# Optimization experiments

Hardware: AMD Instinct MI355X
Metric: run time of the kernel (lower is better)

Reference implementation:

```python
import jax, jax.numpy as jnp
import numpy as np

N = 4096
NODE_DIM = 256
HIDDEN = 64
N_CLASSES = 16
N_HEADS = 4
NEG_SLOPE = 0.01  # F.leaky_relu default


def _xavier(key, shape):
    fan_out, fan_in = shape[0], shape[1]
    limit = float(np.sqrt(6.0 / (fan_in + fan_out)))
    return jax.random.uniform(key, shape, jnp.float32, -limit, limit)


def setup_inputs() -> dict:
    key = jax.random.key(0)
    ks = jax.random.split(key, 8)
    x = jax.random.normal(ks[0], (N, NODE_DIM), jnp.float32)
    adj_mat = jax.random.randint(ks[1], (N, N), 0, 2, jnp.int32)
    # head-stacked layer-1 params
    W1 = _xavier(ks[2], (N_HEADS * HIDDEN, NODE_DIM)).reshape(N_HEADS, HIDDEN, NODE_DIM)
    a1_1 = _xavier(ks[3], (N_HEADS * HIDDEN, 1)).reshape(N_HEADS, HIDDEN)
    a2_1 = _xavier(ks[4], (N_HEADS * HIDDEN, 1)).reshape(N_HEADS, HIDDEN)
    # layer-2 params
    W2 = _xavier(ks[5], (N_CLASSES, N_HEADS * HIDDEN))
    a1_2 = _xavier(ks[6], (N_CLASSES, 1))[:, 0]
    a2_2 = _xavier(ks[7], (N_CLASSES, 1))[:, 0]
    return {"x": x, "adj_mat": adj_mat, "W1": W1, "a1_1": a1_1, "a2_1": a2_1,
            "W2": W2, "a1_2": a1_2, "a2_2": a2_2}


def _attention_layer(x, adj_f, W, a1, a2):
    # x: [N, in_dim], W: [out_dim, in_dim], a1/a2: [out_dim]
    h = x @ W.T                               # [N, d]
    f1 = h @ a1                               # [N]
    f2 = h @ a2                               # [N]
    e = jax.nn.leaky_relu(f1[:, None] + f2[None, :], NEG_SLOPE)  # [N, N]
    e = e * adj_f
    e = jnp.where(e == 0, -jnp.inf, e)        # faithful to torch.where(e==0, -inf, e)
    alpha = jax.nn.softmax(e, axis=1)         # [N, N]
    return alpha @ h                          # [N, d]


def reference(x, adj_mat, W1, a1_1, a2_1, W2, a1_2, a2_2):
    adj_f = adj_mat.astype(x.dtype)
    # layer 1: vmap over heads, concat along feature dim
    heads = jax.vmap(_attention_layer, in_axes=(None, None, 0, 0, 0))(
        x, adj_f, W1, a1_1, a2_1)              # [H, N, hidden]
    h = jnp.transpose(heads, (1, 0, 2)).reshape(N, N_HEADS * HIDDEN)
    h = jax.nn.elu(h)
    # dropout p=0.0 -> identity
    logits = _attention_layer(h, adj_f, W2, a1_2, a2_2)  # [N, n_classes]
    return logits
```

## Files before the change

### kernel.cpp

```cpp
#include <hip/hip_runtime.h>
#include <cstdint>

typedef __bf16 bf16x8 __attribute__((ext_vector_type(8)));
typedef float  f32x4  __attribute__((ext_vector_type(4)));

__device__ __forceinline__ void split8(const float* v, bf16x8& hi, bf16x8& lo) {
    union { bf16x8 v; __bf16 e[8]; } h, l;
    #pragma unroll
    for (int j = 0; j < 8; j++) {
        __bf16 hb = (__bf16)v[j];
        float  r  = v[j] - (float)hb;
        h.e[j] = hb; l.e[j] = (__bf16)r;
    }
    hi = h.v; lo = l.v;
}
__device__ __forceinline__ bf16x8 cvt8(const float* v) {
    union { bf16x8 v; __bf16 e[8]; } u;
    #pragma unroll
    for (int j = 0; j < 8; j++) u.e[j] = (__bf16)v[j];
    return u.v;
}
__device__ __forceinline__ void splitstore(unsigned short* ph, unsigned short* pl, float v) {
    __bf16 hb = (__bf16)v;
    float  r  = v - (float)hb;
    __bf16 lb = (__bf16)r;
    unsigned short hu, lu;
    __builtin_memcpy(&hu, &hb, 2); __builtin_memcpy(&lu, &lb, 2);
    *ph = hu; *pl = lu;
}
__device__ __forceinline__ unsigned short f2bfh(float v) {
    __bf16 hb = (__bf16)v; unsigned short hu;
    __builtin_memcpy(&hu, &hb, 2); return hu;
}

__global__ __launch_bounds__(256)
void kzero(float4* __restrict__ p) {
    p[blockIdx.x * 256 + threadIdx.x] = float4{0.f, 0.f, 0.f, 0.f};
}

__global__ __launch_bounds__(256)
void kpre(const int* __restrict__ adj, unsigned long long* __restrict__ bm64,
          const float* __restrict__ w1, const float* __restrict__ w2,
          unsigned short* __restrict__ w1h, unsigned short* __restrict__ w1l,
          unsigned short* __restrict__ w2h, unsigned short* __restrict__ w2l) {
    int bx = blockIdx.x, tid = threadIdx.x;
    if (bx < 8192) {
        int row = bx >> 1, jbase = (bx & 1) * 2048;
        int wave = tid >> 6, lane = tid & 63;
        const int* base = adj + (size_t)row * 4096 + jbase + wave * 512;
        unsigned long long* bmw = bm64 + row * 64 + (jbase >> 6) + wave * 8;
        #pragma unroll
        for (int it = 0; it < 8; it++) {
            int v = base[it * 64 + lane];
            unsigned long long mask = __ballot(v != 0);
            if (lane == 0) bmw[it] = mask;
        }
        return;
    }
    int e = ((bx - 8192) * 256 + tid) * 4;
    const float* src; unsigned short *dh, *dl;
    if (e < 65536) { src = w1 + e; dh = w1h + e; dl = w1l + e; }
    else { int e2 = e - 65536; src = w2 + e2; dh = w2h + e2; dl = w2l + e2; }
    #pragma unroll
    for (int j = 0; j < 4; j++) splitstore(dh + j, dl + j, src[j]);
}

__global__ __launch_bounds__(256)
void k1_gemm(const float* __restrict__ x,
             const unsigned short* __restrict__ w1h,
             const unsigned short* __restrict__ w1l,
             const float* __restrict__ a11, const float* __restrict__ a21,
             unsigned short* __restrict__ h1t_hi, float* __restrict__ fvals) {
    int tid = threadIdx.x, wave = tid >> 6, lane = tid & 63;
    int q = lane >> 4, m = lane & 15;
    int i0 = blockIdx.x * 16;
    int c0 = wave * 64;
    f32x4 acc[4] = {};
    #pragma unroll
    for (int k0 = 0; k0 < 256; k0 += 32) {
        bf16x8 ah, al;
        split8(x + (i0 + m) * 256 + k0 + q * 8, ah, al);
        #pragma unroll
        for (int ct = 0; ct < 4; ct++) {
            bf16x8 bh = *(const bf16x8*)(w1h + (c0 + ct * 16 + m) * 256 + k0 + q * 8);
            bf16x8 bl = *(const bf16x8*)(w1l + (c0 + ct * 16 + m) * 256 + k0 + q * 8);
            acc[ct] = __builtin_amdgcn_mfma_f32_16x16x32_bf16(ah, bh, acc[ct], 0, 0, 0);
            acc[ct] = __builtin_amdgcn_mfma_f32_16x16x32_bf16(al, bh, acc[ct], 0, 0, 0);
            acc[ct] = __builtin_amdgcn_mfma_f32_16x16x32_bf16(ah, bl, acc[ct], 0, 0, 0);
        }
    }
    float a1v[4], a2v[4];
    #pragma unroll
    for (int ct = 0; ct < 4; ct++) {
        a1v[ct] = a11[wave * 64 + ct * 16 + m];
        a2v[ct] = a21[wave * 64 + ct * 16 + m];
    }
    #pragma unroll
    for (int r = 0; r < 4; r++) {
        int i = i0 + q * 4 + r;
        float s1 = 0.f, s2 = 0.f;
        #pragma unroll
        for (int ct = 0; ct < 4; ct++) {
            int c = c0 + ct * 16 + m;
            h1t_hi[c * 4096 + i] = f2bfh(acc[ct][r]);
            s1 += acc[ct][r] * a1v[ct];
            s2 += acc[ct][r] * a2v[ct];
        }
        #pragma unroll
        for (int off = 1; off < 16; off <<= 1) {
            s1 += __shfl_xor(s1, off);
            s2 += __shfl_xor(s2, off);
        }
        if (m == 0) {
            fvals[wave * 4096 + i] = s1;
            fvals[16384 + wave * 4096 + i] = s2;
        }
    }
}

template<int NCT, int JLEN, bool ATOM>
__global__ __launch_bounds__(256)
void attn_kernel(const unsigned char* __restrict__ bmb,
                 const float* __restrict__ f1_all,
                 const float* __restrict__ f2_all,
                 const unsigned short* __restrict__ BTh_all,
                 float* __restrict__ pacc,
                 float* __restrict__ zacc,
                 int pstride) {
    constexpr int S    = JLEN / 32;
    constexpr int ST   = (S % 8 == 0) ? S + 4 : S;
    constexpr int PR   = S / 4;
    constexpr int NU4  = 128 * PR;
    constexpr int CR   = NCT * 16;
    constexpr int TSTR = 40;
    int tid = threadIdx.x, wave = tid >> 6, lane = tid & 63;
    int q = lane >> 4, m = lane & 15;
    int head = blockIdx.y;
    int i0 = blockIdx.x * 128;
    int jstart = blockIdx.z * JLEN;

    if (!ATOM) {
        pacc += (size_t)blockIdx.z * (size_t)(4096 * pstride);
        zacc += (size_t)blockIdx.z * (size_t)((NCT == 4 ? 4 : 1) * 4096);
    }

    __shared__ unsigned int ldsbm[128 * ST];
    __shared__ unsigned short ldsbt[2][CR * TSTR];

    const unsigned short* BTh = BTh_all + (size_t)head * CR * 4096;

    for (int c = tid; c < NU4; c += 256) {
        int row = c / PR, part = c % PR;
        uint4 v = *(const uint4*)(bmb + (size_t)(i0 + row) * 512 + (jstart >> 3) + part * 16);
        *(uint4*)&ldsbm[row * ST + part * 4] = v;
    }
    uint4 vstage;
    int sc = tid >> 2, sp = tid & 3;
    if (tid < CR * 4) {
        vstage = *(const uint4*)(BTh + (size_t)sc * 4096 + jstart + sp * 8);
        *(uint4*)&ldsbt[0][sc * TSTR + sp * 8] = vstage;
    }

    const float* f1 = f1_all + head * 4096;
    const float* f2 = f2_all + head * 4096;
    int col0 = head * CR;

    int r0 = wave * 32;
    float f1s0 = f1[i0 + r0 + m];
    float f1s1 = f1[i0 + r0 + 16 + m];

    f32x4 acc0[NCT] = {}, acc1[NCT] = {};
    float z0 = 0.f, z1 = 0.f;

    constexpr int NIT = JLEN / 32;
    for (int it = 0; it < NIT; it++) {
        __syncthreads();
        int jl = it * 32;
        if (it + 1 < NIT && tid < CR * 4)
            vstage = *(const uint4*)(BTh + (size_t)sc * 4096 + jstart + jl + 32 + sp * 8);

        unsigned int md0 = ldsbm[(r0 + m) * ST + (jl >> 5)];
        unsigned int md1 = ldsbm[(r0 + 16 + m) * ST + (jl >> 5)];
        const float4* f2p = (const float4*)(f2 + jstart + jl + q * 8);
        float4 fa = f2p[0], fb = f2p[1];
        float fv[8] = {fa.x, fa.y, fa.z, fa.w, fb.x, fb.y, fb.z, fb.w};
        float pv0[8], pv1[8];
        #pragma unroll
        for (int jj = 0; jj < 8; jj++) {
            int bit = q * 8 + jj;
            float s0 = f1s0 + fv[jj];
            float e0 = fmaxf(s0, 0.01f * s0);
            bool v0 = ((md0 >> bit) & 1u) && (s0 != 0.0f);
            float p0 = v0 ? __expf(e0) : 0.0f;
            z0 += p0; pv0[jj] = p0;
            float s1 = f1s1 + fv[jj];
            float e1 = fmaxf(s1, 0.01f * s1);
            bool v1 = ((md1 >> bit) & 1u) && (s1 != 0.0f);
            float p1 = v1 ? __expf(e1) : 0.0f;
            z1 += p1; pv1[jj] = p1;
        }
        bf16x8 ah0 = cvt8(pv0), ah1 = cvt8(pv1);
        int cur = it & 1;
        #pragma unroll
        for (int ct = 0; ct < NCT; ct++) {
            bf16x8 bh = *(const bf16x8*)&ldsbt[cur][(ct * 16 + m) * TSTR + q * 8];
            acc0[ct] = __builtin_amdgcn_mfma_f32_16x16x32_bf16(ah0, bh, acc0[ct], 0, 0, 0);
            acc1[ct] = __builtin_amdgcn_mfma_f32_16x16x32_bf16(ah1, bh, acc1[ct], 0, 0, 0);
        }
        if (it + 1 < NIT && tid < CR * 4)
            *(uint4*)&ldsbt[1 - cur][sc * TSTR + sp * 8] = vstage;
    }
    z0 += __shfl_xor(z0, 16); z0 += __shfl_xor(z0, 32);
    z1 += __shfl_xor(z1, 16); z1 += __shfl_xor(z1, 32);
    if (lane < 16) {
        if (ATOM) {
            atomicAdd(&zacc[head * 4096 + i0 + r0 + lane], z0);
            atomicAdd(&zacc[head * 4096 + i0 + r0 + 16 + lane], z1);
        } else {
            zacc[head * 4096 + i0 + r0 + lane] = z0;
            zacc[head * 4096 + i0 + r0 + 16 + lane] = z1;
        }
    }
    #pragma unroll
    for (int ct = 0; ct < NCT; ct++)
        #pragma unroll
        for (int r = 0; r < 4; r++) {
            int col = col0 + ct * 16 + m;
            int rowA = i0 + r0 + q * 4 + r;
            if (ATOM) {
                atomicAdd(&pacc[rowA * pstride + col], acc0[ct][r]);
                atomicAdd(&pacc[(rowA + 16) * pstride + col], acc1[ct][r]);
            } else {
                pacc[rowA * pstride + col] = acc0[ct][r];
                pacc[(rowA + 16) * pstride + col] = acc1[ct][r];
            }
        }
}

__global__ __launch_bounds__(256)
void fin1c(const float* __restrict__ pp, const float* __restrict__ zp, int nj,
           unsigned short* __restrict__ hh, unsigned short* __restrict__ hl) {
    int row = blockIdx.x, col = threadIdx.x;
    float s = 0.f;
    for (int jc = 0; jc < nj; jc++) s += pp[(size_t)jc * (4096 * 256) + row * 256 + col];
    int head = col >> 6;
    float zz = 0.f;
    for (int jc = 0; jc < nj; jc++) zz += zp[jc * (4 * 4096) + head * 4096 + row];
    float v = s / zz;
    v = (v > 0.f) ? v : (__expf(v) - 1.0f);
    splitstore(&hh[row * 256 + col], &hl[row * 256 + col], v);
}

__global__ __launch_bounds__(256)
void k3_layer2(const unsigned short* __restrict__ helu_hi,
               const unsigned short* __restrict__ helu_lo,
               const unsigned short* __restrict__ w2h,
               const unsigned short* __restrict__ w2l,
               const float* __restrict__ a12,
               const float* __restrict__ a22,
               unsigned short* __restrict__ h2t_hi,
               float* __restrict__ fq) {
    int tid = threadIdx.x, wave = tid >> 6, lane = tid & 63;
    int q = lane >> 4, m = lane & 15;
    int i0 = (blockIdx.x * 4 + wave) * 16;
    f32x4 acc = {};
    #pragma unroll
    for (int k0 = 0; k0 < 256; k0 += 32) {
        bf16x8 ah = *(const bf16x8*)(helu_hi + (i0 + m) * 256 + k0 + q * 8);
        bf16x8 al = *(const bf16x8*)(helu_lo + (i0 + m) * 256 + k0 + q * 8);
        bf16x8 bh = *(const bf16x8*)(w2h + m * 256 + k0 + q * 8);
        bf16x8 bl = *(const bf16x8*)(w2l + m * 256 + k0 + q * 8);
        acc = __builtin_amdgcn_mfma_f32_16x16x32_bf16(ah, bh, acc, 0, 0, 0);
        acc = __builtin_amdgcn_mfma_f32_16x16x32_bf16(al, bh, acc, 0, 0, 0);
        acc = __builtin_amdgcn_mfma_f32_16x16x32_bf16(ah, bl, acc, 0, 0, 0);
    }
    float a1v = a12[m], a2v = a22[m];
    #pragma unroll
    for (int r = 0; r < 4; r++) {
        float v = acc[r];
        int i = i0 + q * 4 + r;
        h2t_hi[m * 4096 + i] = f2bfh(v);
        float s1 = v * a1v, s2 = v * a2v;
        #pragma unroll
        for (int off = 1; off < 16; off <<= 1) {
            s1 += __shfl_xor(s1, off);
            s2 += __shfl_xor(s2, off);
        }
        if (m == 0) { fq[i] = s1; fq[4096 + i] = s2; }
    }
}

__global__ __launch_bounds__(256)
void fin2(const float* __restrict__ pp, const float* __restrict__ zp, int nj,
          float* __restrict__ out) {
    int idx = blockIdx.x * 256 + threadIdx.x;
    float s = 0.f;
    for (int jc = 0; jc < nj; jc++) s += pp[jc * 65536 + idx];
    float zz = 0.f;
    for (int jc = 0; jc < nj; jc++) zz += zp[jc * 4096 + (idx >> 4)];
    out[idx] = s / zz;
}

extern "C" void kernel_launch(void* const* d_in, const int* in_sizes, int n_in,
                              void* d_out, int out_size, void* d_ws, size_t ws_size,
                              hipStream_t stream) {
    const float* x   = (const float*)d_in[0];
    const int*   adj = (const int*)d_in[1];
    const float* w1  = (const float*)d_in[2];
    const float* a11 = (const float*)d_in[3];
    const float* a21 = (const float*)d_in[4];
    const float* w2  = (const float*)d_in[5];
    const float* a12 = (const float*)d_in[6];
    const float* a22 = (const float*)d_in[7];
    float* out = (float*)d_out;

    uint8_t* w = (uint8_t*)d_ws;
    unsigned long long* bm  = (unsigned long long*)(w);
    unsigned short* h1t_hi  = (unsigned short*)(w + (2u << 20));
    unsigned short* h2t_hi  = (unsigned short*)(w + (4u << 20));
    float*          fvals   = (float*)(w + (4u << 20) + (128u << 10));
    float*          fq      = (float*)(w + (4u << 20) + (256u << 10));
    unsigned short* w1h     = (unsigned short*)(w + (4u << 20) + (288u << 10));
    unsigned short* w1l     = (unsigned short*)(w + (4u << 20) + (416u << 10));
    unsigned short* w2h     = (unsigned short*)(w + (4u << 20) + (544u << 10));
    unsigned short* w2l     = (unsigned short*)(w + (4u << 20) + (552u << 10));
    unsigned short* helu_hi = (unsigned short*)(w + (4u << 20) + (560u << 10));
    unsigned short* helu_lo = (unsigned short*)(w + (4u << 20) + (2608u << 10));

    bool big = ws_size >= ((size_t)48 << 20);
    float* p1 = (float*)(w + (9u << 20));
    float *z1, *p2, *z2;
    if (big) {
        z1 = p1 + (size_t)8 * 4096 * 256;
        p2 = z1 + 8 * 4 * 4096;
        z2 = p2 + (size_t)16 * 4096 * 16;
    } else {
        z1 = p1 + 4096 * 256;
        p2 = z1 + 4 * 4096;
        z2 = p2 + 4096 * 16;
    }

    if (!big) kzero<<<1108, 256, 0, stream>>>((float4*)p1);
    kpre<<<8260, 256, 0, stream>>>(adj, bm, w1, w2, w1h, w1l, w2h, w2l);
    k1_gemm<<<256, 256, 0, stream>>>(x, w1h, w1l, a11, a21, h1t_hi, fvals);
    if (big)
        attn_kernel<4, 512, false><<<dim3(32, 4, 8), 256, 0, stream>>>(
            (const unsigned char*)bm, fvals, fvals + 16384, h1t_hi, p1, z1, 256);
    else
        attn_kernel<4, 512, true><<<dim3(32, 4, 8), 256, 0, stream>>>(
            (const unsigned char*)bm, fvals, fvals + 16384, h1t_hi, p1, z1, 256);
    fin1c<<<4096, 256, 0, stream>>>(p1, z1, big ? 8 : 1, helu_hi, helu_lo);
    k3_layer2<<<64, 256, 0, stream>>>(helu_hi, helu_lo, w2h, w2l, a12, a22,
                                      h2t_hi, fq);
    if (big)
        attn_kernel<1, 256, false><<<dim3(32, 1, 16), 256, 0, stream>>>(
            (const unsigned char*)bm, fq, fq + 4096, h2t_hi, p2, z2, 16);
    else
        attn_kernel<1, 256, true><<<dim3(32, 1, 16), 256, 0, stream>>>(
            (const unsigned char*)bm, fq, fq + 4096, h2t_hi, p2, z2, 16);
    fin2<<<256, 256, 0, stream>>>(p2, z2, big ? 16 : 1, out);
}
```

Measured before the change: 201.0 us.

## Fuse layer-1 finalize into layer-2 GEMM, compute softmax denominators via MFMA, use exp2

The layer-1 finalize (partial reduction, normalization, ELU, hi/lo split) now runs inside the layer-2 projection kernel. Results are staged in LDS instead of a global helu buffer, which removes one launch and a global round trip. The attention kernel now gets its row-sum denominators from an extra MFMA against a ones vector instead of scalar adds and shuffles. Logits are pre-scaled by log2(e) so the kernel can use exp2 directly. The fused kernel uses only one wave for its MFMA stage and has low parallelism in the reduction loop, which may cost throughput.

```diff
diff --git a/kernel.cpp b/kernel.cpp
--- a/kernel.cpp
+++ b/kernel.cpp
@@ -3,6 +3,8 @@
 
 typedef __bf16 bf16x8 __attribute__((ext_vector_type(8)));
 typedef float  f32x4  __attribute__((ext_vector_type(4)));
+
+#define LOG2E 1.44269504088896f
 
 __device__ __forceinline__ void split8(const float* v, bf16x8& hi, bf16x8& lo) {
     union { bf16x8 v; __bf16 e[8]; } h, l;
@@ -112,8 +114,8 @@
             s2 += __shfl_xor(s2, off);
         }
         if (m == 0) {
-            fvals[wave * 4096 + i] = s1;
-            fvals[16384 + wave * 4096 + i] = s2;
+            fvals[wave * 4096 + i] = s1 * LOG2E;
+            fvals[16384 + wave * 4096 + i] = s2 * LOG2E;
         }
     }
 }
@@ -169,8 +171,17 @@
     float f1s0 = f1[i0 + r0 + m];
     float f1s1 = f1[i0 + r0 + 16 + m];
 
+    bf16x8 bones;
+    {
+        union { bf16x8 v; unsigned short u[8]; } t;
+        unsigned short one = (m == 0) ? 0x3F80 : 0;
+        #pragma unroll
+        for (int j = 0; j < 8; j++) t.u[j] = one;
+        bones = t.v;
+    }
+
     f32x4 acc0[NCT] = {}, acc1[NCT] = {};
-    float z0 = 0.f, z1 = 0.f;
+    f32x4 accz0 = {}, accz1 = {};
 
     constexpr int NIT = JLEN / 32;
     for (int it = 0; it < NIT; it++) {
@@ -191,13 +202,13 @@
             float s0 = f1s0 + fv[jj];
             float e0 = fmaxf(s0, 0.01f * s0);
             bool v0 = ((md0 >> bit) & 1u) && (s0 != 0.0f);
-            float p0 = v0 ? __expf(e0) : 0.0f;
-            z0 += p0; pv0[jj] = p0;
+            float p0 = v0 ? __builtin_exp2f(e0) : 0.0f;
+            pv0[jj] = p0;
             float s1 = f1s1 + fv[jj];
             float e1 = fmaxf(s1, 0.01f * s1);
             bool v1 = ((md1 >> bit) & 1u) && (s1 != 0.0f);
-            float p1 = v1 ? __expf(e1) : 0.0f;
-            z1 += p1; pv1[jj] = p1;
+            float p1 = v1 ? __builtin_exp2f(e1) : 0.0f;
+            pv1[jj] = p1;
         }
         bf16x8 ah0 = cvt8(pv0), ah1 = cvt8(pv1);
         int cur = it & 1;
@@ -207,18 +218,22 @@
             acc0[ct] = __builtin_amdgcn_mfma_f32_16x16x32_bf16(ah0, bh, acc0[ct], 0, 0, 0);
             acc1[ct] = __builtin_amdgcn_mfma_f32_16x16x32_bf16(ah1, bh, acc1[ct], 0, 0, 0);
         }
+        accz0 = __builtin_amdgcn_mfma_f32_16x16x32_bf16(ah0, bones, accz0, 0, 0, 0);
+        accz1 = __builtin_amdgcn_mfma_f32_16x16x32_bf16(ah1, bones, accz1, 0, 0, 0);
         if (it + 1 < NIT && tid < CR * 4)
             *(uint4*)&ldsbt[1 - cur][sc * TSTR + sp * 8] = vstage;
     }
-    z0 += __shfl_xor(z0, 16); z0 += __shfl_xor(z0, 32);
-    z1 += __shfl_xor(z1, 16); z1 += __shfl_xor(z1, 32);
-    if (lane < 16) {
-        if (ATOM) {
-            atomicAdd(&zacc[head * 4096 + i0 + r0 + lane], z0);
-            atomicAdd(&zacc[head * 4096 + i0 + r0 + 16 + lane], z1);
-        } else {
-            zacc[head * 4096 + i0 + r0 + lane] = z0;
-            zacc[head * 4096 + i0 + r0 + 16 + lane] = z1;
+    if (m == 0) {
+        #pragma unroll
+        for (int r = 0; r < 4; r++) {
+            int rowA = i0 + r0 + q * 4 + r;
+            if (ATOM) {
+                atomicAdd(&zacc[head * 4096 + rowA], accz0[r]);
+                atomicAdd(&zacc[head * 4096 + rowA + 16], accz1[r]);
+            } else {
+                zacc[head * 4096 + rowA] = accz0[r];
+                zacc[head * 4096 + rowA + 16] = accz1[r];
+            }
         }
     }
     #pragma unroll
@@ -238,36 +253,34 @@
 }
 
 __global__ __launch_bounds__(256)
-void fin1c(const float* __restrict__ pp, const float* __restrict__ zp, int nj,
-           unsigned short* __restrict__ hh, unsigned short* __restrict__ hl) {
-    int row = blockIdx.x, col = threadIdx.x;
-    float s = 0.f;
-    for (int jc = 0; jc < nj; jc++) s += pp[(size_t)jc * (4096 * 256) + row * 256 + col];
-    int head = col >> 6;
-    float zz = 0.f;
-    for (int jc = 0; jc < nj; jc++) zz += zp[jc * (4 * 4096) + head * 4096 + row];
-    float v = s / zz;
-    v = (v > 0.f) ? v : (__expf(v) - 1.0f);
-    splitstore(&hh[row * 256 + col], &hl[row * 256 + col], v);
-}
-
-__global__ __launch_bounds__(256)
-void k3_layer2(const unsigned short* __restrict__ helu_hi,
-               const unsigned short* __restrict__ helu_lo,
-               const unsigned short* __restrict__ w2h,
-               const unsigned short* __restrict__ w2l,
-               const float* __restrict__ a12,
-               const float* __restrict__ a22,
-               unsigned short* __restrict__ h2t_hi,
-               float* __restrict__ fq) {
-    int tid = threadIdx.x, wave = tid >> 6, lane = tid & 63;
-    int q = lane >> 4, m = lane & 15;
-    int i0 = (blockIdx.x * 4 + wave) * 16;
+void k3f(const float* __restrict__ pp, const float* __restrict__ zp, int nj,
+         const unsigned short* __restrict__ w2h,
+         const unsigned short* __restrict__ w2l,
+         const float* __restrict__ a12, const float* __restrict__ a22,
+         unsigned short* __restrict__ h2t_hi, float* __restrict__ fq) {
+    constexpr int ASTR = 264;
+    __shared__ unsigned short Ah[16 * ASTR], Al[16 * ASTR];
+    int tid = threadIdx.x;
+    int i0 = blockIdx.x * 16;
+    int head = tid >> 6;
+    for (int r = 0; r < 16; r++) {
+        int row = i0 + r;
+        float s = 0.f;
+        for (int jc = 0; jc < nj; jc++) s += pp[(size_t)jc * (4096 * 256) + row * 256 + tid];
+        float zz = 0.f;
+        for (int jc = 0; jc < nj; jc++) zz += zp[jc * 16384 + head * 4096 + row];
+        float v = s / zz;
+        v = (v > 0.f) ? v : (__expf(v) - 1.0f);
+        splitstore(&Ah[r * ASTR + tid], &Al[r * ASTR + tid], v);
+    }
+    __syncthreads();
+    if (tid >= 64) return;
+    int lane = tid, q = lane >> 4, m = lane & 15;
     f32x4 acc = {};
     #pragma unroll
     for (int k0 = 0; k0 < 256; k0 += 32) {
-        bf16x8 ah = *(const bf16x8*)(helu_hi + (i0 + m) * 256 + k0 + q * 8);
-        bf16x8 al = *(const bf16x8*)(helu_lo + (i0 + m) * 256 + k0 + q * 8);
+        bf16x8 ah = *(const bf16x8*)&Ah[m * ASTR + k0 + q * 8];
+        bf16x8 al = *(const bf16x8*)&Al[m * ASTR + k0 + q * 8];
         bf16x8 bh = *(const bf16x8*)(w2h + m * 256 + k0 + q * 8);
         bf16x8 bl = *(const bf16x8*)(w2l + m * 256 + k0 + q * 8);
         acc = __builtin_amdgcn_mfma_f32_16x16x32_bf16(ah, bh, acc, 0, 0, 0);
@@ -286,7 +299,7 @@
             s1 += __shfl_xor(s1, off);
             s2 += __shfl_xor(s2, off);
         }
-        if (m == 0) { fq[i] = s1; fq[4096 + i] = s2; }
+        if (m == 0) { fq[i] = s1 * LOG2E; fq[4096 + i] = s2 * LOG2E; }
     }
 }
 
@@ -324,11 +337,9 @@
     unsigned short* w1l     = (unsigned short*)(w + (4u << 20) + (416u << 10));
     unsigned short* w2h     = (unsigned short*)(w + (4u << 20) + (544u << 10));
     unsigned short* w2l     = (unsigned short*)(w + (4u << 20) + (552u << 10));
-    unsigned short* helu_hi = (unsigned short*)(w + (4u << 20) + (560u << 10));
-    unsigned short* helu_lo = (unsigned short*)(w + (4u << 20) + (2608u << 10));
 
     bool big = ws_size >= ((size_t)48 << 20);
-    float* p1 = (float*)(w + (9u << 20));
+    float* p1 = (float*)(w + (5u << 20));
     float *z1, *p2, *z2;
     if (big) {
         z1 = p1 + (size_t)8 * 4096 * 256;
@@ -349,9 +360,8 @@
     else
         attn_kernel<4, 512, true><<<dim3(32, 4, 8), 256, 0, stream>>>(
             (const unsigned char*)bm, fvals, fvals + 16384, h1t_hi, p1, z1, 256);
-    fin1c<<<4096, 256, 0, stream>>>(p1, z1, big ? 8 : 1, helu_hi, helu_lo);
-    k3_layer2<<<64, 256, 0, stream>>>(helu_hi, helu_lo, w2h, w2l, a12, a22,
-                                      h2t_hi, fq);
+    k3f<<<256, 256, 0, stream>>>(p1, z1, big ? 8 : 1, w2h, w2l, a12, a22,
+                                 h2t_hi, fq);
     if (big)
         attn_kernel<1, 256, false><<<dim3(32, 1, 16), 256, 0, stream>>>(
             (const unsigned char*)bm, fq, fq + 4096, h2t_hi, p2, z2, 16);
```

Measured after the change: 233.9 us. 1.16x slower.
